# Kernel optimization log

Measured on AMD Instinct MI355X. Metric: run time of the kernel, lower is better.

## Reference

```python
import jax, jax.numpy as jnp
import numpy as np

B, N, D = 2, 8192, 32
RADIUS2 = 0.03 ** 2
SIM_THRESH = 0.7
MIN_LEAF = 10
EPS = 1e-8


def setup_inputs() -> dict:
    key = jax.random.key(0)
    ks = jax.random.split(key, 5)
    # points scaled to [0, 0.4)^3 so the 0.03 radius finds a few neighbors per point
    points = jax.random.uniform(ks[0], (B, N, 3), dtype=jnp.float32) * 0.4
    embeddings = jax.random.normal(ks[1], (B, N, D), dtype=jnp.float32)
    leaf_mask = jax.random.randint(ks[2], (B, N), 0, 2).astype(jnp.int32)
    # consistency_net: Linear(2D -> D), ReLU, Linear(D -> D); stored as (in, out)
    W1 = jax.random.normal(ks[3], (2 * D, D), dtype=jnp.float32) / np.sqrt(2 * D)
    b1 = jnp.zeros((D,), dtype=jnp.float32)
    W2 = jax.random.normal(ks[4], (D, D), dtype=jnp.float32) / np.sqrt(D)
    b2 = jnp.zeros((D,), dtype=jnp.float32)
    return {"points": points, "embeddings": embeddings, "leaf_mask": leaf_mask,
            "W1": W1, "b1": b1, "W2": W2, "b2": b2}


def reference(points, embeddings, leaf_mask, W1, b1, W2, b2):
    leaf = leaf_mask > 0  # [B,N]
    # squared pairwise distances via ||a||^2 + ||b||^2 - 2 a.b (avoids [B,N,N,3])
    sq = jnp.sum(points * points, axis=-1)  # [B,N]
    d2 = sq[:, :, None] + sq[:, None, :] - 2.0 * jnp.einsum('bnc,bmc->bnm', points, points)
    nb = (d2 < RADIUS2) & leaf[:, None, :]  # neighbor j must be a leaf point
    nb_count = jnp.sum(nb, axis=-1)  # includes self when leaf[i]
    # cosine similarity with per-vector norm clamp (torch F.cosine_similarity eps)
    norms = jnp.maximum(jnp.linalg.norm(embeddings, axis=-1, keepdims=True), EPS)
    en = embeddings / norms
    sim = jnp.einsum('bnd,bmd->bnm', en, en)
    similar = nb & (sim > SIM_THRESH)
    cnt = jnp.sum(similar, axis=-1)  # [B,N]
    w = similar.astype(embeddings.dtype)
    mean_sim = jnp.einsum('bnm,bmd->bnd', w, embeddings) / jnp.maximum(cnt, 1)[..., None]
    combined = jnp.concatenate([embeddings, mean_sim], axis=-1)  # [B,N,2D]
    h = jax.nn.relu(combined @ W1 + b1)
    out = h @ W2 + b2
    batch_ok = (jnp.sum(leaf, axis=-1) >= MIN_LEAF)[:, None]  # skip batches with <10 leaves
    cond = leaf & (nb_count > 1) & (cnt > 0) & batch_ok
    return jnp.where(cond[..., None], out, embeddings)
```

## Files before the change

### kernel.cpp

```cpp
#include <hip/hip_runtime.h>

#define NPTS 8192
#define BN   16384
#define D    32
#define R2   0.0009f
#define SIMT 0.7f
#define RAD  0.03f
#define BLOCK 256
#define PBLOCK 1024
#define PWAVES 16
#define ZBINS 512
#define ZSCALE 1280.0f
#define AFIELDS 34

__global__ __launch_bounds__(BLOCK) void histscan_kernel(
    const float* __restrict__ pts, const float* __restrict__ emb,
    const int* __restrict__ leaf, float* __restrict__ invn,
    int* __restrict__ histA, int* __restrict__ histL,
    int* __restrict__ leafcnt, unsigned* __restrict__ done,
    int* __restrict__ rsA, int* __restrict__ rsL,
    int* __restrict__ curA, int* __restrict__ curL) {
  const int p = blockIdx.x * BLOCK + threadIdx.x;
  const float z = pts[3 * p + 2];
  int bin = (int)(z * ZSCALE); if (bin > ZBINS - 1) bin = ZBINS - 1;
  const int b = p >> 13;
  const int lf = leaf[p] > 0;
  atomicAdd(&histA[b * ZBINS + bin], 1);
  if (lf) atomicAdd(&histL[b * ZBINS + bin], 1);

  const float4* er = (const float4*)(emb + (size_t)p * D);
  float ss = 0.f;
#pragma unroll
  for (int i = 0; i < D / 4; ++i) {
    float4 v = er[i];
    ss += v.x * v.x + v.y * v.y + v.z * v.z + v.w * v.w;
  }
  invn[p] = 1.0f / fmaxf(sqrtf(ss), 1e-8f);

  const unsigned long long m = __ballot(lf);
  if ((threadIdx.x & 63) == 0) atomicAdd(&leafcnt[b], (int)__popcll(m));

  __shared__ int islast;
  __threadfence();
  if (threadIdx.x == 0) {
    const unsigned t = __hip_atomic_fetch_add(done, 1u, __ATOMIC_ACQ_REL,
                                              __HIP_MEMORY_SCOPE_AGENT);
    islast = (t == gridDim.x - 1);
  }
  __syncthreads();
  if (!islast) return;

  const int wv = threadIdx.x >> 6;
  const int lane = threadIdx.x & 63;
  const int sb = wv & 1;
  const int* __restrict__ h = (wv < 2) ? histA : histL;
  int* __restrict__ rs = (wv < 2) ? rsA : rsL;
  int* __restrict__ cu = (wv < 2) ? curA : curL;
  int carry = 0;
  for (int c = 0; c < ZBINS / 64; ++c) {
    const int idx = c * 64 + lane;
    const int v = __hip_atomic_load(&h[sb * ZBINS + idx], __ATOMIC_RELAXED,
                                    __HIP_MEMORY_SCOPE_AGENT);
    int incl = v;
#pragma unroll
    for (int off = 1; off < 64; off <<= 1) {
      const int t = __shfl_up(incl, off);
      if (lane >= off) incl += t;
    }
    const int excl = carry + incl - v;
    rs[sb * (ZBINS + 1) + idx] = excl;
    cu[sb * ZBINS + idx] = excl;
    carry += __shfl(incl, 63);
  }
  if (lane == 0) rs[sb * (ZBINS + 1) + ZBINS] = carry;
}

__global__ __launch_bounds__(BLOCK) void scatter_kernel(
    const float* __restrict__ pts, const float* __restrict__ emb,
    const int* __restrict__ leaf, const float* __restrict__ invn,
    int* __restrict__ curA, int* __restrict__ curL,
    float4* __restrict__ sortedA, int* __restrict__ permA,
    float4* __restrict__ pts4L, float* __restrict__ invL,
    float* __restrict__ embL) {
  const int p = blockIdx.x * BLOCK + threadIdx.x;
  const float x = pts[3 * p + 0];
  const float y = pts[3 * p + 1];
  const float z = pts[3 * p + 2];
  const float sq = x * x + y * y + z * z;
  const int lf = leaf[p] > 0;
  const float inv = invn[p];
  int bin = (int)(z * ZSCALE); if (bin > ZBINS - 1) bin = ZBINS - 1;
  const int b = p >> 13;

  const int dst = b * NPTS + atomicAdd(&curA[b * ZBINS + bin], 1);
  sortedA[dst] = make_float4(x, y, z, lf ? inv : -inv);
  permA[dst] = p;

  if (lf) {
    const int dl = b * NPTS + atomicAdd(&curL[b * ZBINS + bin], 1);
    pts4L[dl] = make_float4(x, y, z, 0.5f * (sq - R2));
    invL[dl] = inv;
    const float4* __restrict__ s4 = (const float4*)(emb + (size_t)p * D);
    float4* __restrict__ d4 = (float4*)(embL + (size_t)dl * D);
#pragma unroll
    for (int k = 0; k < D / 4; ++k) d4[k] = s4[k];
  }
}

__global__ __launch_bounds__(PBLOCK) void pair_kernel(
    const float4* __restrict__ sortedA, const int* __restrict__ permA,
    const float4* __restrict__ pts4L, const float* __restrict__ invL,
    const float* __restrict__ embL, const float* __restrict__ emb,
    const int* __restrict__ rsL, const int* __restrict__ leafcnt,
    const float* __restrict__ W1, const float* __restrict__ b1,
    const float* __restrict__ W2, const float* __restrict__ b2,
    float* __restrict__ out) {
  const int ig   = blockIdx.x;
  const int b    = ig >> 7;
  const int lane = threadIdx.x & 63;
  const int wv   = threadIdx.x >> 6;
  const int sg   = ig * 64 + lane;

  __shared__ float red[AFIELDS][64];
  for (int t = threadIdx.x; t < AFIELDS * 64; t += PBLOCK)
    (&red[0][0])[t] = 0.f;
  __syncthreads();

  const float4 A = sortedA[sg];
  const float inv_i = fabsf(A.w);
  const float mhsq = -0.5f * (A.x * A.x + A.y * A.y + A.z * A.z);
  const int p = permA[sg];

  float4 ei[D / 4];
  {
    const float4* __restrict__ e4 = (const float4*)(emb + (size_t)p * D);
#pragma unroll
    for (int k = 0; k < D / 4; ++k) ei[k] = e4[k];
  }

  float zmin = A.z, zmax = A.z;
#pragma unroll
  for (int off = 1; off < 64; off <<= 1) {
    zmin = fminf(zmin, __shfl_xor(zmin, off));
    zmax = fmaxf(zmax, __shfl_xor(zmax, off));
  }
  int klo = (int)((zmin - RAD) * ZSCALE) - 1; if (klo < 0) klo = 0;
  int khi = (int)((zmax + RAD) * ZSCALE) + 1; if (khi > ZBINS - 1) khi = ZBINS - 1;
  klo = __builtin_amdgcn_readfirstlane(klo);
  khi = __builtin_amdgcn_readfirstlane(khi);
  const int jlo = b * NPTS + rsL[b * (ZBINS + 1) + klo];
  const int jhi = b * NPTS + rsL[b * (ZBINS + 1) + khi + 1];
  const int len = jhi - jlo;
  int c0 = jlo + (len * wv) / PWAVES;
  int c1 = jlo + (len * (wv + 1)) / PWAVES;
  c0 = __builtin_amdgcn_readfirstlane(c0);
  c1 = __builtin_amdgcn_readfirstlane(c1);

  float acc[D];
#pragma unroll
  for (int d = 0; d < D; ++d) acc[d] = 0.f;
  float nbc = 0.f, cnt = 0.f;

  auto process = [&](const float4 c, const int jj) {
    const float t = fmaf(A.z, c.z, fmaf(A.y, c.y, fmaf(A.x, c.x, mhsq)));
    if (t > c.w) {
      nbc += 1.0f;
      const float4* __restrict__ ej4 = (const float4*)(embL + (size_t)jj * D);
      float s0 = 0.f, s1 = 0.f, s2 = 0.f, s3 = 0.f;
#pragma unroll
      for (int k = 0; k < D / 4; ++k) {
        const float4 vj = ej4[k];
        s0 = fmaf(ei[k].x, vj.x, s0);
        s1 = fmaf(ei[k].y, vj.y, s1);
        s2 = fmaf(ei[k].z, vj.z, s2);
        s3 = fmaf(ei[k].w, vj.w, s3);
      }
      const float s = ((s0 + s1) + (s2 + s3)) * inv_i * invL[jj];
      if (s > SIMT) {
        cnt += 1.0f;
#pragma unroll
        for (int k = 0; k < D / 4; ++k) {
          const float4 vj = ej4[k];
          acc[4 * k + 0] += vj.x;
          acc[4 * k + 1] += vj.y;
          acc[4 * k + 2] += vj.z;
          acc[4 * k + 3] += vj.w;
        }
      }
    }
  };

  const int nfull = (c1 - c0) & ~7;
  if (nfull > 0) {
    float4 cur[8], nxt[8];
#pragma unroll
    for (int u = 0; u < 8; ++u) cur[u] = pts4L[c0 + u];
    for (int j = c0; j < c0 + nfull; j += 8) {
      const int jn = (j + 8 < c0 + nfull) ? (j + 8) : c0;
#pragma unroll
      for (int u = 0; u < 8; ++u) nxt[u] = pts4L[jn + u];
#pragma unroll
      for (int u = 0; u < 8; ++u) process(cur[u], j + u);
#pragma unroll
      for (int u = 0; u < 8; ++u) cur[u] = nxt[u];
    }
  }
  for (int j = c0 + nfull; j < c1; ++j) process(pts4L[j], j);

  if (nbc != 0.f) atomicAdd(&red[0][lane], nbc);
  if (cnt != 0.f) {
    atomicAdd(&red[1][lane], cnt);
#pragma unroll
    for (int d = 0; d < D; ++d) atomicAdd(&red[2 + d][lane], acc[d]);
  }
  __syncthreads();

  if (threadIdx.x < 64) {
    const float tnbc = red[0][lane];
    const float tcnt = red[1][lane];
    const float rinv = 1.0f / fmaxf(tcnt, 1.0f);

    float e[D];
#pragma unroll
    for (int k = 0; k < D / 4; ++k) {
      e[4 * k + 0] = ei[k].x; e[4 * k + 1] = ei[k].y;
      e[4 * k + 2] = ei[k].z; e[4 * k + 3] = ei[k].w;
    }

    float h[D];
#pragma unroll
    for (int k = 0; k < D; ++k) h[k] = b1[k];
    for (int d = 0; d < D; ++d) {
      const float c = e[d];
      const float* __restrict__ w = W1 + (size_t)d * D;
#pragma unroll
      for (int k = 0; k < D; ++k) h[k] = fmaf(c, w[k], h[k]);
    }
    for (int d = 0; d < D; ++d) {
      const float c = red[2 + d][lane] * rinv;
      const float* __restrict__ w = W1 + (size_t)(D + d) * D;
#pragma unroll
      for (int k = 0; k < D; ++k) h[k] = fmaf(c, w[k], h[k]);
    }
#pragma unroll
    for (int k = 0; k < D; ++k) h[k] = fmaxf(h[k], 0.f);

    float o[D];
#pragma unroll
    for (int m = 0; m < D; ++m) o[m] = b2[m];
    for (int k = 0; k < D; ++k) {
      const float c = h[k];
      const float* __restrict__ w = W2 + (size_t)k * D;
#pragma unroll
      for (int m = 0; m < D; ++m) o[m] = fmaf(c, w[m], o[m]);
    }

    const bool lf = A.w > 0.f;
    const bool cond = lf && (tnbc >= 2.0f) && (tcnt >= 1.0f) && (leafcnt[b] >= 10);

    float4* outr = (float4*)(out + (size_t)p * D);
#pragma unroll
    for (int i = 0; i < D / 4; ++i) {
      float4 v;
      if (cond) { v.x = o[4*i+0]; v.y = o[4*i+1]; v.z = o[4*i+2]; v.w = o[4*i+3]; }
      else      { v = ei[i]; }
      outr[i] = v;
    }
  }
}

extern "C" void kernel_launch(void* const* d_in, const int* in_sizes, int n_in,
                              void* d_out, int out_size, void* d_ws, size_t ws_size,
                              hipStream_t stream) {
  (void)in_sizes; (void)n_in; (void)out_size; (void)ws_size;
  const float* pts  = (const float*)d_in[0];
  const float* emb  = (const float*)d_in[1];
  const int*   leaf = (const int*)d_in[2];
  const float* W1   = (const float*)d_in[3];
  const float* b1   = (const float*)d_in[4];
  const float* W2   = (const float*)d_in[5];
  const float* b2   = (const float*)d_in[6];
  float* out = (float*)d_out;

  char* ws = (char*)d_ws;
  size_t off = 0;
  auto alloc = [&](size_t bytes) { void* r = ws + off; off = (off + bytes + 15) & ~(size_t)15; return r; };

  float4*   sortedA = (float4*)alloc((size_t)BN * 16);
  int*      permA   = (int*)alloc((size_t)BN * 4);
  float4*   pts4L   = (float4*)alloc((size_t)BN * 16);
  float*    invL    = (float*)alloc((size_t)BN * 4);
  float*    embL    = (float*)alloc((size_t)BN * D * 4);
  float*    invn    = (float*)alloc((size_t)BN * 4);
  int*      rsA     = (int*)alloc(2 * (ZBINS + 1) * 4);
  int*      rsL     = (int*)alloc(2 * (ZBINS + 1) * 4);
  int*      curA    = (int*)alloc(2 * ZBINS * 4);
  int*      curL    = (int*)alloc(2 * ZBINS * 4);
  int*      histA   = (int*)alloc(2 * ZBINS * 4);
  int*      histL   = (int*)alloc(2 * ZBINS * 4);
  int*      leafcnt = (int*)alloc(16);
  unsigned* done    = (unsigned*)alloc(16);

  hipMemsetAsync(histA, 0, 2 * (2 * ZBINS * 4) + 32, stream);
  histscan_kernel<<<BN / BLOCK, BLOCK, 0, stream>>>(
      pts, emb, leaf, invn, histA, histL, leafcnt, done, rsA, rsL, curA, curL);
  scatter_kernel<<<BN / BLOCK, BLOCK, 0, stream>>>(
      pts, emb, leaf, invn, curA, curL, sortedA, permA, pts4L, invL, embL);
  pair_kernel<<<BN / 64, PBLOCK, 0, stream>>>(
      sortedA, permA, pts4L, invL, embL, emb, rsL, leafcnt,
      W1, b1, W2, b2, out);
}
```

Before: 124.3 us.

## Fuse histogram, scan, scatter and pair kernels into one persistent kernel with grid barriers

Merges the three launches into a single 256-block kernel that uses atomic-counter grid barriers between the histogram, prefix-scan, scatter and pair phases. Wave 0 of each block handles one 64-point chunk in the early phases and keeps its per-point values in registers, so the invn buffer and its global round-trip go away. This removes launch gaps and inter-kernel drains. In exchange it depends on all 256 blocks of 1024 threads being co-resident, otherwise the spin barriers deadlock, and it leaves most waves idle during the early phases.

```diff
diff --git a/kernel.cpp b/kernel.cpp
--- a/kernel.cpp
+++ b/kernel.cpp
@@ -6,123 +6,112 @@
 #define R2   0.0009f
 #define SIMT 0.7f
 #define RAD  0.03f
-#define BLOCK 256
-#define PBLOCK 1024
+#define TB   1024
+#define GRID 256
 #define PWAVES 16
 #define ZBINS 512
 #define ZSCALE 1280.0f
 #define AFIELDS 34
 
-__global__ __launch_bounds__(BLOCK) void histscan_kernel(
+__device__ __forceinline__ void grid_barrier(unsigned* ctr) {
+  __syncthreads();
+  if (threadIdx.x == 0) {
+    __hip_atomic_fetch_add(ctr, 1u, __ATOMIC_ACQ_REL, __HIP_MEMORY_SCOPE_AGENT);
+    while (__hip_atomic_load(ctr, __ATOMIC_ACQUIRE,
+                             __HIP_MEMORY_SCOPE_AGENT) < (unsigned)GRID)
+      __builtin_amdgcn_s_sleep(1);
+  }
+  __syncthreads();
+}
+
+__global__ __launch_bounds__(TB, 4) void fused_kernel(
     const float* __restrict__ pts, const float* __restrict__ emb,
-    const int* __restrict__ leaf, float* __restrict__ invn,
+    const int* __restrict__ leaf,
+    const float* __restrict__ W1, const float* __restrict__ b1,
+    const float* __restrict__ W2, const float* __restrict__ b2,
+    float* __restrict__ out,
     int* __restrict__ histA, int* __restrict__ histL,
-    int* __restrict__ leafcnt, unsigned* __restrict__ done,
+    int* __restrict__ leafcnt, unsigned* __restrict__ bar,
     int* __restrict__ rsA, int* __restrict__ rsL,
-    int* __restrict__ curA, int* __restrict__ curL) {
-  const int p = blockIdx.x * BLOCK + threadIdx.x;
-  const float z = pts[3 * p + 2];
-  int bin = (int)(z * ZSCALE); if (bin > ZBINS - 1) bin = ZBINS - 1;
-  const int b = p >> 13;
-  const int lf = leaf[p] > 0;
-  atomicAdd(&histA[b * ZBINS + bin], 1);
-  if (lf) atomicAdd(&histL[b * ZBINS + bin], 1);
-
-  const float4* er = (const float4*)(emb + (size_t)p * D);
-  float ss = 0.f;
-#pragma unroll
-  for (int i = 0; i < D / 4; ++i) {
-    float4 v = er[i];
-    ss += v.x * v.x + v.y * v.y + v.z * v.z + v.w * v.w;
-  }
-  invn[p] = 1.0f / fmaxf(sqrtf(ss), 1e-8f);
-
-  const unsigned long long m = __ballot(lf);
-  if ((threadIdx.x & 63) == 0) atomicAdd(&leafcnt[b], (int)__popcll(m));
-
-  __shared__ int islast;
-  __threadfence();
-  if (threadIdx.x == 0) {
-    const unsigned t = __hip_atomic_fetch_add(done, 1u, __ATOMIC_ACQ_REL,
-                                              __HIP_MEMORY_SCOPE_AGENT);
-    islast = (t == gridDim.x - 1);
-  }
-  __syncthreads();
-  if (!islast) return;
-
-  const int wv = threadIdx.x >> 6;
-  const int lane = threadIdx.x & 63;
-  const int sb = wv & 1;
-  const int* __restrict__ h = (wv < 2) ? histA : histL;
-  int* __restrict__ rs = (wv < 2) ? rsA : rsL;
-  int* __restrict__ cu = (wv < 2) ? curA : curL;
-  int carry = 0;
-  for (int c = 0; c < ZBINS / 64; ++c) {
-    const int idx = c * 64 + lane;
-    const int v = __hip_atomic_load(&h[sb * ZBINS + idx], __ATOMIC_RELAXED,
-                                    __HIP_MEMORY_SCOPE_AGENT);
-    int incl = v;
-#pragma unroll
-    for (int off = 1; off < 64; off <<= 1) {
-      const int t = __shfl_up(incl, off);
-      if (lane >= off) incl += t;
-    }
-    const int excl = carry + incl - v;
-    rs[sb * (ZBINS + 1) + idx] = excl;
-    cu[sb * ZBINS + idx] = excl;
-    carry += __shfl(incl, 63);
-  }
-  if (lane == 0) rs[sb * (ZBINS + 1) + ZBINS] = carry;
-}
-
-__global__ __launch_bounds__(BLOCK) void scatter_kernel(
-    const float* __restrict__ pts, const float* __restrict__ emb,
-    const int* __restrict__ leaf, const float* __restrict__ invn,
     int* __restrict__ curA, int* __restrict__ curL,
     float4* __restrict__ sortedA, int* __restrict__ permA,
     float4* __restrict__ pts4L, float* __restrict__ invL,
     float* __restrict__ embL) {
-  const int p = blockIdx.x * BLOCK + threadIdx.x;
-  const float x = pts[3 * p + 0];
-  const float y = pts[3 * p + 1];
-  const float z = pts[3 * p + 2];
-  const float sq = x * x + y * y + z * z;
-  const int lf = leaf[p] > 0;
-  const float inv = invn[p];
-  int bin = (int)(z * ZSCALE); if (bin > ZBINS - 1) bin = ZBINS - 1;
-  const int b = p >> 13;
-
-  const int dst = b * NPTS + atomicAdd(&curA[b * ZBINS + bin], 1);
-  sortedA[dst] = make_float4(x, y, z, lf ? inv : -inv);
-  permA[dst] = p;
-
-  if (lf) {
-    const int dl = b * NPTS + atomicAdd(&curL[b * ZBINS + bin], 1);
-    pts4L[dl] = make_float4(x, y, z, 0.5f * (sq - R2));
-    invL[dl] = inv;
-    const float4* __restrict__ s4 = (const float4*)(emb + (size_t)p * D);
-    float4* __restrict__ d4 = (float4*)(embL + (size_t)dl * D);
-#pragma unroll
-    for (int k = 0; k < D / 4; ++k) d4[k] = s4[k];
-  }
-}
-
-__global__ __launch_bounds__(PBLOCK) void pair_kernel(
-    const float4* __restrict__ sortedA, const int* __restrict__ permA,
-    const float4* __restrict__ pts4L, const float* __restrict__ invL,
-    const float* __restrict__ embL, const float* __restrict__ emb,
-    const int* __restrict__ rsL, const int* __restrict__ leafcnt,
-    const float* __restrict__ W1, const float* __restrict__ b1,
-    const float* __restrict__ W2, const float* __restrict__ b2,
-    float* __restrict__ out) {
-  const int ig   = blockIdx.x;
-  const int b    = ig >> 7;
   const int lane = threadIdx.x & 63;
   const int wv   = threadIdx.x >> 6;
-  const int sg   = ig * 64 + lane;
+  const int ig   = blockIdx.x;
 
   __shared__ float red[AFIELDS][64];
-  for (int t = threadIdx.x; t < AFIELDS * 64; t += PBLOCK)
+
+  float px = 0.f, py = 0.f, pz = 0.f, psq = 0.f, pinv = 0.f;
+  int pbin = 0, plf = 0, pp = 0, pb = 0;
+  if (wv == 0) {
+    pp = ig * 64 + lane;
+    px = pts[3 * pp + 0]; py = pts[3 * pp + 1]; pz = pts[3 * pp + 2];
+    psq = px * px + py * py + pz * pz;
+    pb = pp >> 13;
+    plf = leaf[pp] > 0;
+    pbin = (int)(pz * ZSCALE); if (pbin > ZBINS - 1) pbin = ZBINS - 1;
+    atomicAdd(&histA[pb * ZBINS + pbin], 1);
+    if (plf) atomicAdd(&histL[pb * ZBINS + pbin], 1);
+    float ss = 0.f;
+    const float4* __restrict__ er = (const float4*)(emb + (size_t)pp * D);
+#pragma unroll
+    for (int k = 0; k < D / 4; ++k) {
+      float4 v = er[k];
+      ss += v.x * v.x + v.y * v.y + v.z * v.z + v.w * v.w;
+    }
+    pinv = 1.0f / fmaxf(sqrtf(ss), 1e-8f);
+    const unsigned long long m = __ballot(plf);
+    if (lane == 0) atomicAdd(&leafcnt[pb], (int)__popcll(m));
+  }
+  grid_barrier(&bar[0]);
+
+  if (ig == 0 && wv < 4) {
+    const int sb = wv & 1;
+    const int* __restrict__ h = (wv < 2) ? histA : histL;
+    int* __restrict__ rs = (wv < 2) ? rsA : rsL;
+    int* __restrict__ cu = (wv < 2) ? curA : curL;
+    int carry = 0;
+    for (int c = 0; c < ZBINS / 64; ++c) {
+      const int idx = c * 64 + lane;
+      const int v = __hip_atomic_load(&h[sb * ZBINS + idx], __ATOMIC_RELAXED,
+                                      __HIP_MEMORY_SCOPE_AGENT);
+      int incl = v;
+#pragma unroll
+      for (int off = 1; off < 64; off <<= 1) {
+        const int t = __shfl_up(incl, off);
+        if (lane >= off) incl += t;
+      }
+      const int excl = carry + incl - v;
+      rs[sb * (ZBINS + 1) + idx] = excl;
+      cu[sb * ZBINS + idx] = excl;
+      carry += __shfl(incl, 63);
+    }
+    if (lane == 0) rs[sb * (ZBINS + 1) + ZBINS] = carry;
+  }
+  grid_barrier(&bar[1]);
+
+  if (wv == 0) {
+    const int dst = pb * NPTS + atomicAdd(&curA[pb * ZBINS + pbin], 1);
+    sortedA[dst] = make_float4(px, py, pz, plf ? pinv : -pinv);
+    permA[dst] = pp;
+    if (plf) {
+      const int dl = pb * NPTS + atomicAdd(&curL[pb * ZBINS + pbin], 1);
+      pts4L[dl] = make_float4(px, py, pz, 0.5f * (psq - R2));
+      invL[dl] = pinv;
+      const float4* __restrict__ s4 = (const float4*)(emb + (size_t)pp * D);
+      float4* __restrict__ d4 = (float4*)(embL + (size_t)dl * D);
+#pragma unroll
+      for (int k = 0; k < D / 4; ++k) d4[k] = s4[k];
+    }
+  }
+  grid_barrier(&bar[2]);
+
+  const int b = ig >> 7;
+  const int sg = ig * 64 + lane;
+
+  for (int t = threadIdx.x; t < AFIELDS * 64; t += TB)
     (&red[0][0])[t] = 0.f;
   __syncthreads();
 
@@ -286,27 +275,25 @@
   size_t off = 0;
   auto alloc = [&](size_t bytes) { void* r = ws + off; off = (off + bytes + 15) & ~(size_t)15; return r; };
 
+  int*      histA   = (int*)alloc(2 * ZBINS * 4);
+  int*      histL   = (int*)alloc(2 * ZBINS * 4);
+  int*      leafcnt = (int*)alloc(16);
+  unsigned* bar     = (unsigned*)alloc(16);
+  const size_t zbytes = off;
+
+  int*      rsA     = (int*)alloc(2 * (ZBINS + 1) * 4);
+  int*      rsL     = (int*)alloc(2 * (ZBINS + 1) * 4);
+  int*      curA    = (int*)alloc(2 * ZBINS * 4);
+  int*      curL    = (int*)alloc(2 * ZBINS * 4);
   float4*   sortedA = (float4*)alloc((size_t)BN * 16);
   int*      permA   = (int*)alloc((size_t)BN * 4);
   float4*   pts4L   = (float4*)alloc((size_t)BN * 16);
   float*    invL    = (float*)alloc((size_t)BN * 4);
   float*    embL    = (float*)alloc((size_t)BN * D * 4);
-  float*    invn    = (float*)alloc((size_t)BN * 4);
-  int*      rsA     = (int*)alloc(2 * (ZBINS + 1) * 4);
-  int*      rsL     = (int*)alloc(2 * (ZBINS + 1) * 4);
-  int*      curA    = (int*)alloc(2 * ZBINS * 4);
-  int*      curL    = (int*)alloc(2 * ZBINS * 4);
-  int*      histA   = (int*)alloc(2 * ZBINS * 4);
-  int*      histL   = (int*)alloc(2 * ZBINS * 4);
-  int*      leafcnt = (int*)alloc(16);
-  unsigned* done    = (unsigned*)alloc(16);
-
-  hipMemsetAsync(histA, 0, 2 * (2 * ZBINS * 4) + 32, stream);
-  histscan_kernel<<<BN / BLOCK, BLOCK, 0, stream>>>(
-      pts, emb, leaf, invn, histA, histL, leafcnt, done, rsA, rsL, curA, curL);
-  scatter_kernel<<<BN / BLOCK, BLOCK, 0, stream>>>(
-      pts, emb, leaf, invn, curA, curL, sortedA, permA, pts4L, invL, embL);
-  pair_kernel<<<BN / 64, PBLOCK, 0, stream>>>(
-      sortedA, permA, pts4L, invL, embL, emb, rsL, leafcnt,
-      W1, b1, W2, b2, out);
+
+  hipMemsetAsync(histA, 0, zbytes, stream);
+  fused_kernel<<<GRID, TB, 0, stream>>>(
+      pts, emb, leaf, W1, b1, W2, b2, out,
+      histA, histL, leafcnt, bar, rsA, rsL, curA, curL,
+      sortedA, permA, pts4L, invL, embL);
 }
```

After: 260.2 us. 109% more time.

## Fuse scatter into pair kernel using a software grid barrier

Applied to the files above, without the earlier changes.

Merges the scatter kernel into the pair kernel. Wave 0 of each of the 256 persistent blocks scatters its 64 points, then all blocks meet at an atomic-counter grid barrier before the pair phase. This removes one kernel launch and its inter-kernel gap. In exchange, correctness relies on all 256 blocks of 1024 threads being co-resident; if they are not, the barrier deadlocks. Spinning blocks also sit idle while waiting.

```diff
diff --git a/kernel.cpp b/kernel.cpp
--- a/kernel.cpp
+++ b/kernel.cpp
@@ -7,11 +7,24 @@
 #define SIMT 0.7f
 #define RAD  0.03f
 #define BLOCK 256
-#define PBLOCK 1024
+#define TB   1024
+#define GRID 256
 #define PWAVES 16
 #define ZBINS 512
 #define ZSCALE 1280.0f
 #define AFIELDS 34
+
+__device__ __forceinline__ void grid_barrier(unsigned* ctr) {
+  __syncthreads();
+  if (threadIdx.x == 0) {
+    __hip_atomic_fetch_add(ctr, 1u, __ATOMIC_RELEASE, __HIP_MEMORY_SCOPE_AGENT);
+    while (__hip_atomic_load(ctr, __ATOMIC_RELAXED,
+                             __HIP_MEMORY_SCOPE_AGENT) < (unsigned)GRID)
+      __builtin_amdgcn_s_sleep(8);
+    (void)__hip_atomic_load(ctr, __ATOMIC_ACQUIRE, __HIP_MEMORY_SCOPE_AGENT);
+  }
+  __syncthreads();
+}
 
 __global__ __launch_bounds__(BLOCK) void histscan_kernel(
     const float* __restrict__ pts, const float* __restrict__ emb,
@@ -75,57 +88,52 @@
   if (lane == 0) rs[sb * (ZBINS + 1) + ZBINS] = carry;
 }
 
-__global__ __launch_bounds__(BLOCK) void scatter_kernel(
+__global__ __launch_bounds__(TB, 4) void sppair_kernel(
     const float* __restrict__ pts, const float* __restrict__ emb,
     const int* __restrict__ leaf, const float* __restrict__ invn,
     int* __restrict__ curA, int* __restrict__ curL,
-    float4* __restrict__ sortedA, int* __restrict__ permA,
-    float4* __restrict__ pts4L, float* __restrict__ invL,
-    float* __restrict__ embL) {
-  const int p = blockIdx.x * BLOCK + threadIdx.x;
-  const float x = pts[3 * p + 0];
-  const float y = pts[3 * p + 1];
-  const float z = pts[3 * p + 2];
-  const float sq = x * x + y * y + z * z;
-  const int lf = leaf[p] > 0;
-  const float inv = invn[p];
-  int bin = (int)(z * ZSCALE); if (bin > ZBINS - 1) bin = ZBINS - 1;
-  const int b = p >> 13;
-
-  const int dst = b * NPTS + atomicAdd(&curA[b * ZBINS + bin], 1);
-  sortedA[dst] = make_float4(x, y, z, lf ? inv : -inv);
-  permA[dst] = p;
-
-  if (lf) {
-    const int dl = b * NPTS + atomicAdd(&curL[b * ZBINS + bin], 1);
-    pts4L[dl] = make_float4(x, y, z, 0.5f * (sq - R2));
-    invL[dl] = inv;
-    const float4* __restrict__ s4 = (const float4*)(emb + (size_t)p * D);
-    float4* __restrict__ d4 = (float4*)(embL + (size_t)dl * D);
-#pragma unroll
-    for (int k = 0; k < D / 4; ++k) d4[k] = s4[k];
-  }
-}
-
-__global__ __launch_bounds__(PBLOCK) void pair_kernel(
-    const float4* __restrict__ sortedA, const int* __restrict__ permA,
-    const float4* __restrict__ pts4L, const float* __restrict__ invL,
-    const float* __restrict__ embL, const float* __restrict__ emb,
     const int* __restrict__ rsL, const int* __restrict__ leafcnt,
     const float* __restrict__ W1, const float* __restrict__ b1,
     const float* __restrict__ W2, const float* __restrict__ b2,
+    float4* __restrict__ sortedA, int* __restrict__ permA,
+    float4* __restrict__ pts4L, float* __restrict__ invL,
+    float* __restrict__ embL, unsigned* __restrict__ bar,
     float* __restrict__ out) {
+  const int lane = threadIdx.x & 63;
+  const int wv   = threadIdx.x >> 6;
   const int ig   = blockIdx.x;
   const int b    = ig >> 7;
-  const int lane = threadIdx.x & 63;
-  const int wv   = threadIdx.x >> 6;
-  const int sg   = ig * 64 + lane;
 
   __shared__ float red[AFIELDS][64];
-  for (int t = threadIdx.x; t < AFIELDS * 64; t += PBLOCK)
+  for (int t = threadIdx.x; t < AFIELDS * 64; t += TB)
     (&red[0][0])[t] = 0.f;
-  __syncthreads();
-
+
+  if (wv == 0) {
+    const int p = ig * 64 + lane;
+    const float x = pts[3 * p + 0];
+    const float y = pts[3 * p + 1];
+    const float z = pts[3 * p + 2];
+    const float sq = x * x + y * y + z * z;
+    const int lf = leaf[p] > 0;
+    const float inv = invn[p];
+    int bin = (int)(z * ZSCALE); if (bin > ZBINS - 1) bin = ZBINS - 1;
+
+    const int dst = b * NPTS + atomicAdd(&curA[b * ZBINS + bin], 1);
+    sortedA[dst] = make_float4(x, y, z, lf ? inv : -inv);
+    permA[dst] = p;
+    if (lf) {
+      const int dl = b * NPTS + atomicAdd(&curL[b * ZBINS + bin], 1);
+      pts4L[dl] = make_float4(x, y, z, 0.5f * (sq - R2));
+      invL[dl] = inv;
+      const float4* __restrict__ s4 = (const float4*)(emb + (size_t)p * D);
+      float4* __restrict__ d4 = (float4*)(embL + (size_t)dl * D);
+#pragma unroll
+      for (int k = 0; k < D / 4; ++k) d4[k] = s4[k];
+    }
+  }
+  grid_barrier(bar);
+
+  const int sg = ig * 64 + lane;
   const float4 A = sortedA[sg];
   const float inv_i = fabsf(A.w);
   const float mhsq = -0.5f * (A.x * A.x + A.y * A.y + A.z * A.z);
@@ -286,27 +294,28 @@
   size_t off = 0;
   auto alloc = [&](size_t bytes) { void* r = ws + off; off = (off + bytes + 15) & ~(size_t)15; return r; };
 
+  int*      histA   = (int*)alloc(2 * ZBINS * 4);
+  int*      histL   = (int*)alloc(2 * ZBINS * 4);
+  int*      leafcnt = (int*)alloc(16);
+  unsigned* done    = (unsigned*)alloc(16);
+  unsigned* bar     = (unsigned*)alloc(16);
+  const size_t zbytes = off;
+
+  int*      rsA     = (int*)alloc(2 * (ZBINS + 1) * 4);
+  int*      rsL     = (int*)alloc(2 * (ZBINS + 1) * 4);
+  int*      curA    = (int*)alloc(2 * ZBINS * 4);
+  int*      curL    = (int*)alloc(2 * ZBINS * 4);
+  float*    invn    = (float*)alloc((size_t)BN * 4);
   float4*   sortedA = (float4*)alloc((size_t)BN * 16);
   int*      permA   = (int*)alloc((size_t)BN * 4);
   float4*   pts4L   = (float4*)alloc((size_t)BN * 16);
   float*    invL    = (float*)alloc((size_t)BN * 4);
   float*    embL    = (float*)alloc((size_t)BN * D * 4);
-  float*    invn    = (float*)alloc((size_t)BN * 4);
-  int*      rsA     = (int*)alloc(2 * (ZBINS + 1) * 4);
-  int*      rsL     = (int*)alloc(2 * (ZBINS + 1) * 4);
-  int*      curA    = (int*)alloc(2 * ZBINS * 4);
-  int*      curL    = (int*)alloc(2 * ZBINS * 4);
-  int*      histA   = (int*)alloc(2 * ZBINS * 4);
-  int*      histL   = (int*)alloc(2 * ZBINS * 4);
-  int*      leafcnt = (int*)alloc(16);
-  unsigned* done    = (unsigned*)alloc(16);
-
-  hipMemsetAsync(histA, 0, 2 * (2 * ZBINS * 4) + 32, stream);
+
+  hipMemsetAsync(histA, 0, zbytes, stream);
   histscan_kernel<<<BN / BLOCK, BLOCK, 0, stream>>>(
       pts, emb, leaf, invn, histA, histL, leafcnt, done, rsA, rsL, curA, curL);
-  scatter_kernel<<<BN / BLOCK, BLOCK, 0, stream>>>(
-      pts, emb, leaf, invn, curA, curL, sortedA, permA, pts4L, invL, embL);
-  pair_kernel<<<BN / 64, PBLOCK, 0, stream>>>(
-      sortedA, permA, pts4L, invL, embL, emb, rsL, leafcnt,
-      W1, b1, W2, b2, out);
+  sppair_kernel<<<GRID, TB, 0, stream>>>(
+      pts, emb, leaf, invn, curA, curL, rsL, leafcnt,
+      W1, b1, W2, b2, sortedA, permA, pts4L, invL, embL, bar, out);
 }
```

New measurement: 246.7 us. +98.4%, slower.
